# Kernel tuning notes

Hardware: AMD Instinct MI355X
Metric: run time of the kernel (lower is better)

## Reference

```python
import jax, jax.numpy as jnp
import numpy as np
import math

N = 2048       # num_nodes (dense graph)
F_IN = 256     # num_in_features
F_OUT = 256    # num_out_features
H = 8          # num_heads
LN_EPS = 1e-5

# NOTE: every e3nn FullyConnectedTensorProduct in this module maps
# (Fx0e) x irreps_sh -> (Kx0e). Only the l=0 spherical-harmonic component can
# couple scalars to scalars, and Y_0 = 1 under normalization='component'.
# Each TP is therefore exactly a linear map with a 1/sqrt(fan_in) path norm,
# and edge_direction does not enter the math at all.


def setup_inputs() -> dict:
    key = jax.random.key(0)
    ks = jax.random.split(key, 12)
    inv = 1.0 / np.sqrt(F_IN)
    return {
        "node_features": jax.random.normal(ks[0], (N, F_IN), jnp.float32),
        "edges_features_distance": jax.random.uniform(ks[1], (N, N), jnp.float32),
        "edges_features_bond": jax.random.uniform(ks[2], (N, N), jnp.float32),
        "edge_direction": jax.random.normal(ks[3], (N * N, 3), jnp.float32),
        "degree_matrix": jax.random.randint(ks[4], (N, N), 0, 2).astype(jnp.float32),
        # tensor-product weights (xavier-ish scale)
        "Wq": jax.random.normal(ks[5], (F_IN, H), jnp.float32) * inv,
        "Wk": jax.random.normal(ks[6], (F_IN, H), jnp.float32) * inv,
        "Wv": jax.random.normal(ks[7], (F_IN, F_OUT), jnp.float32) * inv,
        "w_bond": jax.random.normal(ks[8], (), jnp.float32),
        "w_bond_contrib": jax.random.normal(ks[9], (), jnp.float32),
        "w_gauss": jax.random.normal(ks[10], (), jnp.float32),
    }


def reference(node_features, edges_features_distance, edges_features_bond,
              edge_direction, degree_matrix, Wq, Wk, Wv,
              w_bond, w_bond_contrib, w_gauss):
    scale = 1.0 / jnp.sqrt(jnp.asarray(F_IN, node_features.dtype))
    # scalar-only tensor products == scaled linears (Y_0 = 1)
    q = (node_features @ Wq) * scale              # [N, H]
    k = (node_features @ Wk) * scale              # [N, H]
    v = (node_features @ Wv) * scale              # [N, F_OUT]

    # raw_attention[i,j,h] = (q_i + k_i)/sqrt(H)  (key.transpose(0,1) picks node i)
    qk = (q + k) / math.sqrt(H)                   # [N, H]
    bond = edges_features_bond * (w_bond * w_bond_contrib)   # [N, N]
    gauss = edges_features_distance * w_gauss                 # [N, N]
    raw = qk[:, None, :] + (bond + gauss)[:, :, None]          # [N, N, H]

    mask = jnp.where(degree_matrix > 0, 0.0, -1e9).astype(raw.dtype)
    scores = jax.nn.leaky_relu(raw, 0.2) + mask[:, :, None]
    # torch F.softmax without dim on a 3-D tensor -> dim=0
    attn = jax.nn.softmax(scores, axis=0)          # [N, N, H]
    # F.dropout treated as identity (eval / deterministic baseline)
    attn_mean = attn.mean(axis=2)                  # [N, N]

    # aggregated[i] = sum_j attn_mean[i,j] * v_j  (value[i,j,:] = v(node_j))
    aggregated = attn_mean @ v                     # [N, F_OUT]
    updated_nodes = jax.nn.elu(aggregated)

    # no_grad connectivity update
    un = jax.lax.stop_gradient(updated_nodes)
    sim = un @ un.T                                # [N, N]
    dd = -jax.lax.stop_gradient(edges_features_distance)
    conn = jax.nn.sigmoid(sim) * dd * jax.lax.stop_gradient(degree_matrix)
    mu = conn.mean(axis=-1, keepdims=True)
    var = conn.var(axis=-1, keepdims=True)
    conn = (conn - mu) * jax.lax.rsqrt(var + LN_EPS)
    conn = conn + conn.T
    return updated_nodes, conn
```

## Files before the change

### kernel.cpp

```cpp
#include <hip/hip_runtime.h>
#include <hip/hip_bf16.h>

#define NN 2048
#define FIN 256
#define FOUT 256
#define HH 8

typedef short bhalf8 __attribute__((ext_vector_type(8)));
typedef float f32x4  __attribute__((ext_vector_type(4)));

__device__ __forceinline__ unsigned short f2b(float f) {
    __hip_bfloat16 h = __float2bfloat16(f);
    return *reinterpret_cast<unsigned short*>(&h);
}
__device__ __forceinline__ float b2f(unsigned short u) {
    __hip_bfloat16 h = *reinterpret_cast<__hip_bfloat16*>(&u);
    return __bfloat162float(h);
}

__global__ __launch_bounds__(256) void k1_qkv(
    const float* __restrict__ x, const float* __restrict__ Wq,
    const float* __restrict__ Wk, const float* __restrict__ Wv,
    float* __restrict__ v, float* __restrict__ qk)
{
    const int ib = blockIdx.x * 4;
    const int t  = threadIdx.x;
    __shared__ float xs[4][FIN];
    __shared__ float part[256];
    #pragma unroll
    for (int n = 0; n < 4; ++n) xs[n][t] = x[(long)(ib+n)*FIN + t];
    __syncthreads();
    float a0 = 0.f, a1 = 0.f, a2 = 0.f, a3 = 0.f;
    #pragma unroll 4
    for (int c = 0; c < FIN; ++c) {
        const float wv = Wv[c*FOUT + t];
        a0 = fmaf(xs[0][c], wv, a0); a1 = fmaf(xs[1][c], wv, a1);
        a2 = fmaf(xs[2][c], wv, a2); a3 = fmaf(xs[3][c], wv, a3);
    }
    v[(ib+0)*FOUT + t] = a0 * 0.0625f;
    v[(ib+1)*FOUT + t] = a1 * 0.0625f;
    v[(ib+2)*FOUT + t] = a2 * 0.0625f;
    v[(ib+3)*FOUT + t] = a3 * 0.0625f;
    {
        const int n = t >> 6, h = t & 7, seg = (t >> 3) & 7;
        float a = 0.f;
        for (int c = seg*32; c < seg*32 + 32; ++c)
            a = fmaf(xs[n][c], Wq[c*HH + h] + Wk[c*HH + h], a);
        part[t] = a;
    }
    __syncthreads();
    if (t < 32) {
        const int n = t >> 3, h = t & 7;
        float a = 0.f;
        #pragma unroll
        for (int s2 = 0; s2 < 8; ++s2) a += part[n*64 + s2*8 + h];
        qk[(ib+n)*HH + h] = a * (0.0625f * 0.35355339059327373f);
    }
}

__global__ __launch_bounds__(256) void k1b_vT(
    const float* __restrict__ v, unsigned short* __restrict__ vtb)
{
    const int k0 = blockIdx.x * 64;
    const int f0 = blockIdx.y * 64;
    const int t  = threadIdx.x;
    __shared__ float LT[64][68];
    const int r  = t >> 4;
    const int c4 = (t & 15) * 4;
    #pragma unroll
    for (int p = 0; p < 4; ++p) {
        const float4 q = *(const float4*)&v[(k0 + r + p*16)*FOUT + f0 + c4];
        LT[c4+0][r + p*16] = q.x; LT[c4+1][r + p*16] = q.y;
        LT[c4+2][r + p*16] = q.z; LT[c4+3][r + p*16] = q.w;
    }
    __syncthreads();
    #pragma unroll
    for (int p = 0; p < 4; ++p) {
        const int fr = r + p*16;
        ushort4 ub;
        ub.x = f2b(LT[fr][c4+0]); ub.y = f2b(LT[fr][c4+1]);
        ub.z = f2b(LT[fr][c4+2]); ub.w = f2b(LT[fr][c4+3]);
        *(ushort4*)&vtb[(long)(f0 + fr)*NN + k0 + c4] = ub;
    }
}

__global__ __launch_bounds__(256) void k2_denom(
    const float* __restrict__ bond, const float* __restrict__ dist,
    const float* __restrict__ deg, const float* __restrict__ qk,
    const float* __restrict__ wb, const float* __restrict__ wbc,
    const float* __restrict__ wg, float* __restrict__ D,
    unsigned short* __restrict__ fbuf, unsigned short* __restrict__ ddb)
{
    const float cb = wb[0] * wbc[0];
    const float cg = wg[0];
    const int t  = threadIdx.x;
    const int tx = t & 63;
    const int ty = t >> 6;
    const int j0 = blockIdx.x * 256;
    const int i0 = blockIdx.y * 64;
    const int j  = j0 + tx*4;
    __shared__ float qs[64*8];
    __shared__ float red[4][2048];
    for (int p = t; p < 512; p += 256) qs[p] = qk[i0*8 + p];
    __syncthreads();
    float acc[4][8];
    #pragma unroll
    for (int jj = 0; jj < 4; ++jj)
        #pragma unroll
        for (int h = 0; h < 8; ++h) acc[jj][h] = 0.f;
    const int ibase = i0 + ty*16;
    for (int ii = 0; ii < 16; ++ii) {
        const long idx = (long)(ibase + ii)*NN + j;
        const float4 dv = *(const float4*)&dist[idx];
        const float4 bv = *(const float4*)&bond[idx];
        const float4 gv = *(const float4*)&deg[idx];
        ushort4 fb, db;
        fb.x = f2b((gv.x > 0.f) ? fmaf(cb, bv.x, cg*dv.x) : -__builtin_inff());
        fb.y = f2b((gv.y > 0.f) ? fmaf(cb, bv.y, cg*dv.y) : -__builtin_inff());
        fb.z = f2b((gv.z > 0.f) ? fmaf(cb, bv.z, cg*dv.z) : -__builtin_inff());
        fb.w = f2b((gv.w > 0.f) ? fmaf(cb, bv.w, cg*dv.w) : -__builtin_inff());
        db.x = f2b(-dv.x * gv.x); db.y = f2b(-dv.y * gv.y);
        db.z = f2b(-dv.z * gv.z); db.w = f2b(-dv.w * gv.w);
        *(ushort4*)&fbuf[idx] = fb;
        *(ushort4*)&ddb[idx]  = db;
        float s[4];
        s[0] = b2f(fb.x); s[1] = b2f(fb.y); s[2] = b2f(fb.z); s[3] = b2f(fb.w);
        const float* qrow = &qs[(ty*16 + ii)*8];
        #pragma unroll
        for (int h = 0; h < 8; ++h) {
            const float q = qrow[h];
            #pragma unroll
            for (int jj = 0; jj < 4; ++jj) {
                float r = q + s[jj];
                r = fmaxf(r, 0.2f*r);
                acc[jj][h] += __expf(r);
            }
        }
    }
    #pragma unroll
    for (int jj = 0; jj < 4; ++jj)
        #pragma unroll
        for (int h = 0; h < 8; ++h) red[ty][(tx*4 + jj)*8 + h] = acc[jj][h];
    __syncthreads();
    for (int p = t; p < 2048; p += 256) {
        const float ssum = red[0][p] + red[1][p] + red[2][p] + red[3][p];
        atomicAdd(&D[j0*8 + p], ssum);
    }
}

__global__ __launch_bounds__(256) void k3_attnmean(
    const unsigned short* __restrict__ fbuf, const float* __restrict__ qk,
    const float* __restrict__ D, unsigned short* __restrict__ amb)
{
    const int t  = threadIdx.x;
    const int tx = t & 63;
    const int ty = t >> 6;
    const int j0 = blockIdx.x * 256;
    const int i0 = blockIdx.y * 64;
    const int j  = j0 + tx*4;
    __shared__ float qs[64*8];
    for (int p = t; p < 512; p += 256) qs[p] = qk[i0*8 + p];
    __syncthreads();
    float invD[4][8];
    #pragma unroll
    for (int jj = 0; jj < 4; ++jj) {
        const float4 d0 = *(const float4*)&D[(j + jj)*8 + 0];
        const float4 d1 = *(const float4*)&D[(j + jj)*8 + 4];
        invD[jj][0] = 0.125f / fmaxf(d0.x, 1e-30f);
        invD[jj][1] = 0.125f / fmaxf(d0.y, 1e-30f);
        invD[jj][2] = 0.125f / fmaxf(d0.z, 1e-30f);
        invD[jj][3] = 0.125f / fmaxf(d0.w, 1e-30f);
        invD[jj][4] = 0.125f / fmaxf(d1.x, 1e-30f);
        invD[jj][5] = 0.125f / fmaxf(d1.y, 1e-30f);
        invD[jj][6] = 0.125f / fmaxf(d1.z, 1e-30f);
        invD[jj][7] = 0.125f / fmaxf(d1.w, 1e-30f);
    }
    const int ibase = i0 + ty*16;
    for (int ii = 0; ii < 16; ++ii) {
        const long idx = (long)(ibase + ii)*NN + j;
        const ushort4 fb = *(const ushort4*)&fbuf[idx];
        float s[4];
        s[0] = b2f(fb.x); s[1] = b2f(fb.y); s[2] = b2f(fb.z); s[3] = b2f(fb.w);
        float o[4] = {0.f, 0.f, 0.f, 0.f};
        const float* qrow = &qs[(ty*16 + ii)*8];
        #pragma unroll
        for (int h = 0; h < 8; ++h) {
            const float q = qrow[h];
            #pragma unroll
            for (int jj = 0; jj < 4; ++jj) {
                float r = q + s[jj];
                r = fmaxf(r, 0.2f*r);
                o[jj] = fmaf(__expf(r), invD[jj][h], o[jj]);
            }
        }
        ushort4 ob;
        ob.x = f2b(o[0]); ob.y = f2b(o[1]); ob.z = f2b(o[2]); ob.w = f2b(o[3]);
        *(ushort4*)&amb[idx] = ob;
    }
}

__global__ __launch_bounds__(128) void k4_aggr(
    const unsigned short* __restrict__ amb,
    const unsigned short* __restrict__ vtb,
    float* __restrict__ out0, unsigned short* __restrict__ unb)
{
    const int i0 = blockIdx.x * 32;
    const int f0 = blockIdx.y * 32;
    const int w  = threadIdx.x >> 6;
    const int l  = threadIdx.x & 63;
    const int lm = l & 15, lq = l >> 4;
    const int iw = i0 + w*16;
    f32x4 acc0 = {0,0,0,0}, acc1 = {0,0,0,0};
    const unsigned short* arow  = &amb[(long)(iw + lm)*NN + lq*8];
    const unsigned short* brow0 = &vtb[(long)(f0 + lm)*NN + lq*8];
    const unsigned short* brow1 = &vtb[(long)(f0 + 16 + lm)*NN + lq*8];
    #pragma unroll 4
    for (int kk = 0; kk < NN; kk += 32) {
        const bhalf8 a  = *(const bhalf8*)&arow[kk];
        const bhalf8 b0 = *(const bhalf8*)&brow0[kk];
        const bhalf8 b1 = *(const bhalf8*)&brow1[kk];
        acc0 = __builtin_amdgcn_mfma_f32_16x16x32_bf16(a, b0, acc0, 0, 0, 0);
        acc1 = __builtin_amdgcn_mfma_f32_16x16x32_bf16(a, b1, acc1, 0, 0, 0);
    }
    #pragma unroll
    for (int r = 0; r < 4; ++r) {
        const int i = iw + lq*4 + r;
        float s0 = acc0[r], s1 = acc1[r];
        s0 = (s0 > 0.f) ? s0 : (__expf(s0) - 1.f);
        s1 = (s1 > 0.f) ? s1 : (__expf(s1) - 1.f);
        out0[(long)i*FOUT + f0 + lm]      = s0;
        out0[(long)i*FOUT + f0 + 16 + lm] = s1;
        unb[(long)i*FOUT + f0 + lm]       = f2b(s0);
        unb[(long)i*FOUT + f0 + 16 + lm]  = f2b(s1);
    }
}

__global__ __launch_bounds__(256) void k5_sim(
    const unsigned short* __restrict__ unb, const unsigned short* __restrict__ ddb,
    unsigned short* __restrict__ c0,
    float* __restrict__ rowsum, float* __restrict__ rowsq)
{
    const int i0 = blockIdx.y * 64;
    const int j0 = blockIdx.x * 64;
    const int w  = threadIdx.x >> 6;
    const int l  = threadIdx.x & 63;
    const int lm = l & 15, lq = l >> 4;
    const int iw = i0 + w*16;
    f32x4 acc[4] = {f32x4{0,0,0,0}, f32x4{0,0,0,0}, f32x4{0,0,0,0}, f32x4{0,0,0,0}};
    for (int kk = 0; kk < FOUT; kk += 32) {
        const bhalf8 a = *(const bhalf8*)&unb[(long)(iw + lm)*FOUT + kk + lq*8];
        #pragma unroll
        for (int c = 0; c < 4; ++c) {
            const bhalf8 b = *(const bhalf8*)&unb[(long)(j0 + c*16 + lm)*FOUT + kk + lq*8];
            acc[c] = __builtin_amdgcn_mfma_f32_16x16x32_bf16(a, b, acc[c], 0, 0, 0);
        }
    }
    float srow[4] = {0.f,0.f,0.f,0.f}, qrow[4] = {0.f,0.f,0.f,0.f};
    #pragma unroll
    for (int c = 0; c < 4; ++c) {
        #pragma unroll
        for (int r = 0; r < 4; ++r) {
            const int i = iw + lq*4 + r;
            const int j = j0 + c*16 + lm;
            const long idx = (long)i*NN + j;
            const float sg = 1.f / (1.f + __expf(-acc[c][r]));
            const float val = sg * b2f(ddb[idx]);
            c0[idx] = f2b(val);
            srow[r] += val;
            qrow[r] = fmaf(val, val, qrow[r]);
        }
    }
    #pragma unroll
    for (int r = 0; r < 4; ++r) {
        #pragma unroll
        for (int m = 8; m >= 1; m >>= 1) {
            srow[r] += __shfl_xor(srow[r], m, 64);
            qrow[r] += __shfl_xor(qrow[r], m, 64);
        }
        if (lm == 0) {
            atomicAdd(&rowsum[iw + lq*4 + r], srow[r]);
            atomicAdd(&rowsq[iw + lq*4 + r],  qrow[r]);
        }
    }
}

__global__ void k6_stats(const float* __restrict__ rowsum,
                         const float* __restrict__ rowsq,
                         float* __restrict__ mu, float* __restrict__ rs)
{
    const int i = blockIdx.x*256 + threadIdx.x;
    if (i < NN) {
        const float m = rowsum[i] * (1.f/NN);
        const float var = rowsq[i] * (1.f/NN) - m*m;
        mu[i] = m;
        rs[i] = rsqrtf(var + 1e-5f);
    }
}

__global__ __launch_bounds__(256) void k7_conn(
    const unsigned short* __restrict__ c0, const float* __restrict__ mu,
    const float* __restrict__ rs, float* __restrict__ out1)
{
    const int i0 = blockIdx.y * 64;
    const int j0 = blockIdx.x * 64;
    const int t  = threadIdx.x;
    __shared__ float LT[64][68];
    __shared__ float muj[64], rsj[64];
    const int r  = t >> 4;
    const int c4 = (t & 15) * 4;
    if (t < 64)        muj[t] = mu[j0 + t];
    else if (t < 128)  rsj[t-64] = rs[j0 + t - 64];
    #pragma unroll
    for (int p = 0; p < 4; ++p) {
        const int jl = r + p*16;
        const ushort4 q = *(const ushort4*)&c0[(long)(j0 + jl)*NN + i0 + c4];
        LT[c4+0][jl] = b2f(q.x); LT[c4+1][jl] = b2f(q.y);
        LT[c4+2][jl] = b2f(q.z); LT[c4+3][jl] = b2f(q.w);
    }
    __syncthreads();
    #pragma unroll
    for (int p = 0; p < 4; ++p) {
        const int rr = r + p*16;
        const int i  = i0 + rr;
        const ushort4 xb = *(const ushort4*)&c0[(long)i*NN + j0 + c4];
        const float mi = mu[i], ri = rs[i];
        float4 o;
        o.x = (b2f(xb.x) - mi)*ri + (LT[rr][c4+0] - muj[c4+0])*rsj[c4+0];
        o.y = (b2f(xb.y) - mi)*ri + (LT[rr][c4+1] - muj[c4+1])*rsj[c4+1];
        o.z = (b2f(xb.z) - mi)*ri + (LT[rr][c4+2] - muj[c4+2])*rsj[c4+2];
        o.w = (b2f(xb.w) - mi)*ri + (LT[rr][c4+3] - muj[c4+3])*rsj[c4+3];
        *(float4*)&out1[(long)i*NN + j0 + c4] = o;
    }
}

extern "C" void kernel_launch(void* const* d_in, const int* in_sizes, int n_in,
                              void* d_out, int out_size, void* d_ws, size_t ws_size,
                              hipStream_t stream)
{
    const float* x    = (const float*)d_in[0];
    const float* dist = (const float*)d_in[1];
    const float* bond = (const float*)d_in[2];
    const float* deg  = (const float*)d_in[4];
    const float* Wq   = (const float*)d_in[5];
    const float* Wk   = (const float*)d_in[6];
    const float* Wv   = (const float*)d_in[7];
    const float* wb   = (const float*)d_in[8];
    const float* wbc  = (const float*)d_in[9];
    const float* wg   = (const float*)d_in[10];

    float* out0 = (float*)d_out;
    float* out1 = out0 + (size_t)NN*FOUT;

    char* w = (char*)d_ws;
    unsigned short* fbuf = (unsigned short*)(w);
    unsigned short* c0   = (unsigned short*)(w);
    unsigned short* amb  = (unsigned short*)(w +  8388608);
    unsigned short* ddb  = (unsigned short*)(w + 16777216);
    float* v       = (float*)(w + 33554432);
    unsigned short* vtb = (unsigned short*)(w + 35651584);
    unsigned short* unb = (unsigned short*)(w + 36700160);
    float* qk      = (float*)(w + 37748736);
    float* D       = (float*)(w + 37814272);
    float* rowsum  = (float*)(w + 37879808);
    float* rowsq   = (float*)(w + 37888000);
    float* mu      = (float*)(w + 37896192);
    float* rs      = (float*)(w + 37904384);

    hipMemsetAsync(D, 0, 65536 + 8192 + 8192, stream);

    k1_qkv<<<NN/4, 256, 0, stream>>>(x, Wq, Wk, Wv, v, qk);
    dim3 g1b(NN/64, FOUT/64);
    k1b_vT<<<g1b, 256, 0, stream>>>(v, vtb);
    dim3 g23(NN/256, NN/64);
    k2_denom<<<g23, 256, 0, stream>>>(bond, dist, deg, qk, wb, wbc, wg, D, fbuf, ddb);
    k3_attnmean<<<g23, 256, 0, stream>>>(fbuf, qk, D, amb);
    dim3 g4(NN/32, FOUT/32);
    k4_aggr<<<g4, 128, 0, stream>>>(amb, vtb, out0, unb);
    dim3 g5(NN/64, NN/64);
    k5_sim<<<g5, 256, 0, stream>>>(unb, ddb, c0, rowsum, rowsq);
    k6_stats<<<8, 256, 0, stream>>>(rowsum, rowsq, mu, rs);
    k7_conn<<<g5, 256, 0, stream>>>(c0, mu, rs, out1);
}
```

Measured before the change: 250.8 us.

## Fuse all stages into one persistent kernel with grid-wide barriers

Replaces the eight separate kernel launches with a single persistent kernel of 256 blocks × 1024 threads that runs each stage in turn, separated by atomic-counter grid barriers. It also writes v directly as transposed bf16, dropping the transpose kernel and its buffer, zeroes the accumulators inside the kernel, and folds the stats kernel into the final normalize stage. The aim is to remove launch gaps and intermediate traffic. In exchange, every stage is limited to a fixed grid and pays barrier spin costs, and correctness depends on all 256 blocks being resident at once.

```diff
diff --git a/kernel.cpp b/kernel.cpp
--- a/kernel.cpp
+++ b/kernel.cpp
@@ -5,6 +5,8 @@
 #define FIN 256
 #define FOUT 256
 #define HH 8
+#define NB 256
+#define NT 1024
 
 typedef short bhalf8 __attribute__((ext_vector_type(8)));
 typedef float f32x4  __attribute__((ext_vector_type(4)));
@@ -18,318 +20,309 @@
     return __bfloat162float(h);
 }
 
-__global__ __launch_bounds__(256) void k1_qkv(
-    const float* __restrict__ x, const float* __restrict__ Wq,
-    const float* __restrict__ Wk, const float* __restrict__ Wv,
-    float* __restrict__ v, float* __restrict__ qk)
+__device__ __forceinline__ void gridbar(unsigned* bar, unsigned target) {
+    __syncthreads();
+    if (threadIdx.x == 0) {
+        __threadfence();
+        __hip_atomic_fetch_add(bar, 1u, __ATOMIC_ACQ_REL, __HIP_MEMORY_SCOPE_AGENT);
+        while (__hip_atomic_load(bar, __ATOMIC_ACQUIRE, __HIP_MEMORY_SCOPE_AGENT) < target) {
+            __builtin_amdgcn_s_sleep(8);
+        }
+        __threadfence();
+    }
+    __syncthreads();
+}
+
+union SharedU {
+    struct { float xs[4][4][256]; float part[4][256]; } p1;
+    struct { float qs[512]; float red[4][4][16][4][8]; } p2;
+    struct { float qs[512]; } p3;
+    struct { float LT[64][68]; float mui[64], rii[64], muj[64], rsj[64]; } p7;
+};
+
+__global__ __launch_bounds__(NT, 4) void mega(
+    const float* __restrict__ x,    const float* __restrict__ dist,
+    const float* __restrict__ bond, const float* __restrict__ deg,
+    const float* __restrict__ Wq,   const float* __restrict__ Wk,
+    const float* __restrict__ Wv,   const float* __restrict__ wb,
+    const float* __restrict__ wbc,  const float* __restrict__ wg,
+    float* __restrict__ out0, float* __restrict__ out1,
+    unsigned short* __restrict__ fbuf_c0,
+    unsigned short* __restrict__ amb, unsigned short* __restrict__ ddb,
+    unsigned short* __restrict__ vtb, unsigned short* __restrict__ unb,
+    float* __restrict__ qk, float* __restrict__ D,
+    float* __restrict__ rowsum, float* __restrict__ rowsq,
+    unsigned* __restrict__ bar)
 {
-    const int ib = blockIdx.x * 4;
-    const int t  = threadIdx.x;
-    __shared__ float xs[4][FIN];
-    __shared__ float part[256];
-    #pragma unroll
-    for (int n = 0; n < 4; ++n) xs[n][t] = x[(long)(ib+n)*FIN + t];
-    __syncthreads();
-    float a0 = 0.f, a1 = 0.f, a2 = 0.f, a3 = 0.f;
-    #pragma unroll 4
-    for (int c = 0; c < FIN; ++c) {
-        const float wv = Wv[c*FOUT + t];
-        a0 = fmaf(xs[0][c], wv, a0); a1 = fmaf(xs[1][c], wv, a1);
-        a2 = fmaf(xs[2][c], wv, a2); a3 = fmaf(xs[3][c], wv, a3);
-    }
-    v[(ib+0)*FOUT + t] = a0 * 0.0625f;
-    v[(ib+1)*FOUT + t] = a1 * 0.0625f;
-    v[(ib+2)*FOUT + t] = a2 * 0.0625f;
-    v[(ib+3)*FOUT + t] = a3 * 0.0625f;
+    __shared__ SharedU sh;
+    const int gid = blockIdx.x;
+    const int tid = threadIdx.x;
+
+    if (gid < 128) {
+        const int g = tid >> 8, sub = tid & 255;
+        const int ib = (gid*4 + g) * 4;
+        float (*xs)[256] = sh.p1.xs[g];
+        #pragma unroll
+        for (int n = 0; n < 4; ++n) xs[n][sub] = x[(long)(ib+n)*FIN + sub];
+        __syncthreads();
+        float a0 = 0.f, a1 = 0.f, a2 = 0.f, a3 = 0.f;
+        #pragma unroll 4
+        for (int c = 0; c < FIN; ++c) {
+            const float wv = Wv[c*FOUT + sub];
+            a0 = fmaf(xs[0][c], wv, a0); a1 = fmaf(xs[1][c], wv, a1);
+            a2 = fmaf(xs[2][c], wv, a2); a3 = fmaf(xs[3][c], wv, a3);
+        }
+        ushort4 uv;
+        uv.x = f2b(a0 * 0.0625f); uv.y = f2b(a1 * 0.0625f);
+        uv.z = f2b(a2 * 0.0625f); uv.w = f2b(a3 * 0.0625f);
+        *(ushort4*)&vtb[(long)sub*NN + ib] = uv;
+        {
+            const int n = sub >> 6, h = sub & 7, seg = (sub >> 3) & 7;
+            float a = 0.f;
+            for (int c = seg*32; c < seg*32 + 32; ++c)
+                a = fmaf(xs[n][c], Wq[c*HH + h] + Wk[c*HH + h], a);
+            sh.p1.part[g][sub] = a;
+        }
+        __syncthreads();
+        if (sub < 32) {
+            const int n = sub >> 3, h = sub & 7;
+            float a = 0.f;
+            #pragma unroll
+            for (int s2 = 0; s2 < 8; ++s2) a += sh.p1.part[g][n*64 + s2*8 + h];
+            qk[(ib+n)*HH + h] = a * (0.0625f * 0.35355339059327373f);
+        }
+    } else {
+        const int tp = (gid - 128)*NT + tid;
+        if      (tp < 16384) D[tp] = 0.f;
+        else if (tp < 18432) rowsum[tp - 16384] = 0.f;
+        else if (tp < 20480) rowsq [tp - 18432] = 0.f;
+    }
+    gridbar(bar, NB*1);
+
     {
-        const int n = t >> 6, h = t & 7, seg = (t >> 3) & 7;
-        float a = 0.f;
-        for (int c = seg*32; c < seg*32 + 32; ++c)
-            a = fmaf(xs[n][c], Wq[c*HH + h] + Wk[c*HH + h], a);
-        part[t] = a;
-    }
-    __syncthreads();
-    if (t < 32) {
-        const int n = t >> 3, h = t & 7;
-        float a = 0.f;
-        #pragma unroll
-        for (int s2 = 0; s2 < 8; ++s2) a += part[n*64 + s2*8 + h];
-        qk[(ib+n)*HH + h] = a * (0.0625f * 0.35355339059327373f);
-    }
-}
-
-__global__ __launch_bounds__(256) void k1b_vT(
-    const float* __restrict__ v, unsigned short* __restrict__ vtb)
-{
-    const int k0 = blockIdx.x * 64;
-    const int f0 = blockIdx.y * 64;
-    const int t  = threadIdx.x;
-    __shared__ float LT[64][68];
-    const int r  = t >> 4;
-    const int c4 = (t & 15) * 4;
-    #pragma unroll
-    for (int p = 0; p < 4; ++p) {
-        const float4 q = *(const float4*)&v[(k0 + r + p*16)*FOUT + f0 + c4];
-        LT[c4+0][r + p*16] = q.x; LT[c4+1][r + p*16] = q.y;
-        LT[c4+2][r + p*16] = q.z; LT[c4+3][r + p*16] = q.w;
-    }
-    __syncthreads();
-    #pragma unroll
-    for (int p = 0; p < 4; ++p) {
-        const int fr = r + p*16;
-        ushort4 ub;
-        ub.x = f2b(LT[fr][c4+0]); ub.y = f2b(LT[fr][c4+1]);
-        ub.z = f2b(LT[fr][c4+2]); ub.w = f2b(LT[fr][c4+3]);
-        *(ushort4*)&vtb[(long)(f0 + fr)*NN + k0 + c4] = ub;
-    }
-}
-
-__global__ __launch_bounds__(256) void k2_denom(
-    const float* __restrict__ bond, const float* __restrict__ dist,
-    const float* __restrict__ deg, const float* __restrict__ qk,
-    const float* __restrict__ wb, const float* __restrict__ wbc,
-    const float* __restrict__ wg, float* __restrict__ D,
-    unsigned short* __restrict__ fbuf, unsigned short* __restrict__ ddb)
-{
-    const float cb = wb[0] * wbc[0];
-    const float cg = wg[0];
-    const int t  = threadIdx.x;
-    const int tx = t & 63;
-    const int ty = t >> 6;
-    const int j0 = blockIdx.x * 256;
-    const int i0 = blockIdx.y * 64;
-    const int j  = j0 + tx*4;
-    __shared__ float qs[64*8];
-    __shared__ float red[4][2048];
-    for (int p = t; p < 512; p += 256) qs[p] = qk[i0*8 + p];
-    __syncthreads();
-    float acc[4][8];
-    #pragma unroll
-    for (int jj = 0; jj < 4; ++jj)
-        #pragma unroll
-        for (int h = 0; h < 8; ++h) acc[jj][h] = 0.f;
-    const int ibase = i0 + ty*16;
-    for (int ii = 0; ii < 16; ++ii) {
-        const long idx = (long)(ibase + ii)*NN + j;
-        const float4 dv = *(const float4*)&dist[idx];
-        const float4 bv = *(const float4*)&bond[idx];
-        const float4 gv = *(const float4*)&deg[idx];
-        ushort4 fb, db;
-        fb.x = f2b((gv.x > 0.f) ? fmaf(cb, bv.x, cg*dv.x) : -__builtin_inff());
-        fb.y = f2b((gv.y > 0.f) ? fmaf(cb, bv.y, cg*dv.y) : -__builtin_inff());
-        fb.z = f2b((gv.z > 0.f) ? fmaf(cb, bv.z, cg*dv.z) : -__builtin_inff());
-        fb.w = f2b((gv.w > 0.f) ? fmaf(cb, bv.w, cg*dv.w) : -__builtin_inff());
-        db.x = f2b(-dv.x * gv.x); db.y = f2b(-dv.y * gv.y);
-        db.z = f2b(-dv.z * gv.z); db.w = f2b(-dv.w * gv.w);
-        *(ushort4*)&fbuf[idx] = fb;
-        *(ushort4*)&ddb[idx]  = db;
-        float s[4];
-        s[0] = b2f(fb.x); s[1] = b2f(fb.y); s[2] = b2f(fb.z); s[3] = b2f(fb.w);
-        const float* qrow = &qs[(ty*16 + ii)*8];
-        #pragma unroll
-        for (int h = 0; h < 8; ++h) {
-            const float q = qrow[h];
-            #pragma unroll
-            for (int jj = 0; jj < 4; ++jj) {
-                float r = q + s[jj];
-                r = fmaxf(r, 0.2f*r);
-                acc[jj][h] += __expf(r);
-            }
-        }
-    }
-    #pragma unroll
-    for (int jj = 0; jj < 4; ++jj)
-        #pragma unroll
-        for (int h = 0; h < 8; ++h) red[ty][(tx*4 + jj)*8 + h] = acc[jj][h];
-    __syncthreads();
-    for (int p = t; p < 2048; p += 256) {
-        const float ssum = red[0][p] + red[1][p] + red[2][p] + red[3][p];
-        atomicAdd(&D[j0*8 + p], ssum);
-    }
-}
-
-__global__ __launch_bounds__(256) void k3_attnmean(
-    const unsigned short* __restrict__ fbuf, const float* __restrict__ qk,
-    const float* __restrict__ D, unsigned short* __restrict__ amb)
-{
-    const int t  = threadIdx.x;
-    const int tx = t & 63;
-    const int ty = t >> 6;
-    const int j0 = blockIdx.x * 256;
-    const int i0 = blockIdx.y * 64;
-    const int j  = j0 + tx*4;
-    __shared__ float qs[64*8];
-    for (int p = t; p < 512; p += 256) qs[p] = qk[i0*8 + p];
-    __syncthreads();
-    float invD[4][8];
-    #pragma unroll
-    for (int jj = 0; jj < 4; ++jj) {
-        const float4 d0 = *(const float4*)&D[(j + jj)*8 + 0];
-        const float4 d1 = *(const float4*)&D[(j + jj)*8 + 4];
-        invD[jj][0] = 0.125f / fmaxf(d0.x, 1e-30f);
-        invD[jj][1] = 0.125f / fmaxf(d0.y, 1e-30f);
-        invD[jj][2] = 0.125f / fmaxf(d0.z, 1e-30f);
-        invD[jj][3] = 0.125f / fmaxf(d0.w, 1e-30f);
-        invD[jj][4] = 0.125f / fmaxf(d1.x, 1e-30f);
-        invD[jj][5] = 0.125f / fmaxf(d1.y, 1e-30f);
-        invD[jj][6] = 0.125f / fmaxf(d1.z, 1e-30f);
-        invD[jj][7] = 0.125f / fmaxf(d1.w, 1e-30f);
-    }
-    const int ibase = i0 + ty*16;
-    for (int ii = 0; ii < 16; ++ii) {
-        const long idx = (long)(ibase + ii)*NN + j;
-        const ushort4 fb = *(const ushort4*)&fbuf[idx];
-        float s[4];
-        s[0] = b2f(fb.x); s[1] = b2f(fb.y); s[2] = b2f(fb.z); s[3] = b2f(fb.w);
-        float o[4] = {0.f, 0.f, 0.f, 0.f};
-        const float* qrow = &qs[(ty*16 + ii)*8];
-        #pragma unroll
-        for (int h = 0; h < 8; ++h) {
-            const float q = qrow[h];
-            #pragma unroll
-            for (int jj = 0; jj < 4; ++jj) {
-                float r = q + s[jj];
-                r = fmaxf(r, 0.2f*r);
-                o[jj] = fmaf(__expf(r), invD[jj][h], o[jj]);
-            }
-        }
-        ushort4 ob;
-        ob.x = f2b(o[0]); ob.y = f2b(o[1]); ob.z = f2b(o[2]); ob.w = f2b(o[3]);
-        *(ushort4*)&amb[idx] = ob;
-    }
-}
-
-__global__ __launch_bounds__(128) void k4_aggr(
-    const unsigned short* __restrict__ amb,
-    const unsigned short* __restrict__ vtb,
-    float* __restrict__ out0, unsigned short* __restrict__ unb)
-{
-    const int i0 = blockIdx.x * 32;
-    const int f0 = blockIdx.y * 32;
-    const int w  = threadIdx.x >> 6;
-    const int l  = threadIdx.x & 63;
-    const int lm = l & 15, lq = l >> 4;
-    const int iw = i0 + w*16;
-    f32x4 acc0 = {0,0,0,0}, acc1 = {0,0,0,0};
-    const unsigned short* arow  = &amb[(long)(iw + lm)*NN + lq*8];
-    const unsigned short* brow0 = &vtb[(long)(f0 + lm)*NN + lq*8];
-    const unsigned short* brow1 = &vtb[(long)(f0 + 16 + lm)*NN + lq*8];
-    #pragma unroll 4
-    for (int kk = 0; kk < NN; kk += 32) {
-        const bhalf8 a  = *(const bhalf8*)&arow[kk];
-        const bhalf8 b0 = *(const bhalf8*)&brow0[kk];
-        const bhalf8 b1 = *(const bhalf8*)&brow1[kk];
-        acc0 = __builtin_amdgcn_mfma_f32_16x16x32_bf16(a, b0, acc0, 0, 0, 0);
-        acc1 = __builtin_amdgcn_mfma_f32_16x16x32_bf16(a, b1, acc1, 0, 0, 0);
-    }
-    #pragma unroll
-    for (int r = 0; r < 4; ++r) {
-        const int i = iw + lq*4 + r;
-        float s0 = acc0[r], s1 = acc1[r];
-        s0 = (s0 > 0.f) ? s0 : (__expf(s0) - 1.f);
-        s1 = (s1 > 0.f) ? s1 : (__expf(s1) - 1.f);
-        out0[(long)i*FOUT + f0 + lm]      = s0;
-        out0[(long)i*FOUT + f0 + 16 + lm] = s1;
-        unb[(long)i*FOUT + f0 + lm]       = f2b(s0);
-        unb[(long)i*FOUT + f0 + 16 + lm]  = f2b(s1);
-    }
-}
-
-__global__ __launch_bounds__(256) void k5_sim(
-    const unsigned short* __restrict__ unb, const unsigned short* __restrict__ ddb,
-    unsigned short* __restrict__ c0,
-    float* __restrict__ rowsum, float* __restrict__ rowsq)
-{
-    const int i0 = blockIdx.y * 64;
-    const int j0 = blockIdx.x * 64;
-    const int w  = threadIdx.x >> 6;
-    const int l  = threadIdx.x & 63;
-    const int lm = l & 15, lq = l >> 4;
-    const int iw = i0 + w*16;
-    f32x4 acc[4] = {f32x4{0,0,0,0}, f32x4{0,0,0,0}, f32x4{0,0,0,0}, f32x4{0,0,0,0}};
-    for (int kk = 0; kk < FOUT; kk += 32) {
-        const bhalf8 a = *(const bhalf8*)&unb[(long)(iw + lm)*FOUT + kk + lq*8];
+        const float cb = wb[0] * wbc[0];
+        const float cg = wg[0];
+        const int bx = gid & 7, by = gid >> 3;
+        const int j0 = bx*256, i0 = by*64;
+        const int w  = tid >> 6, lane = tid & 63;
+        const int jb = w & 3,  tqh = w >> 2;
+        const int jq = lane & 15, tql = lane >> 4;
+        const int tq = tqh*4 + tql;
+        const int j  = j0 + (jb*16 + jq)*4;
+        if (tid < 512) sh.p2.qs[tid] = qk[i0*8 + tid];
+        __syncthreads();
+        float acc[4][8];
+        #pragma unroll
+        for (int jj = 0; jj < 4; ++jj)
+            #pragma unroll
+            for (int h = 0; h < 8; ++h) acc[jj][h] = 0.f;
+        #pragma unroll
+        for (int ii = 0; ii < 4; ++ii) {
+            const int i = i0 + tq*4 + ii;
+            const long idx = (long)i*NN + j;
+            const float4 dv = *(const float4*)&dist[idx];
+            const float4 bv = *(const float4*)&bond[idx];
+            const float4 gv = *(const float4*)&deg[idx];
+            ushort4 fb, db;
+            fb.x = f2b((gv.x > 0.f) ? fmaf(cb, bv.x, cg*dv.x) : -__builtin_inff());
+            fb.y = f2b((gv.y > 0.f) ? fmaf(cb, bv.y, cg*dv.y) : -__builtin_inff());
+            fb.z = f2b((gv.z > 0.f) ? fmaf(cb, bv.z, cg*dv.z) : -__builtin_inff());
+            fb.w = f2b((gv.w > 0.f) ? fmaf(cb, bv.w, cg*dv.w) : -__builtin_inff());
+            db.x = f2b(-dv.x * gv.x); db.y = f2b(-dv.y * gv.y);
+            db.z = f2b(-dv.z * gv.z); db.w = f2b(-dv.w * gv.w);
+            *(ushort4*)&fbuf_c0[idx] = fb;
+            *(ushort4*)&ddb[idx]     = db;
+            float s[4];
+            s[0] = b2f(fb.x); s[1] = b2f(fb.y); s[2] = b2f(fb.z); s[3] = b2f(fb.w);
+            const float* qrow = &sh.p2.qs[(tq*4 + ii)*8];
+            #pragma unroll
+            for (int h = 0; h < 8; ++h) {
+                const float q = qrow[h];
+                #pragma unroll
+                for (int jj = 0; jj < 4; ++jj) {
+                    float r = q + s[jj];
+                    r = fmaxf(r, 0.2f*r);
+                    acc[jj][h] += __expf(r);
+                }
+            }
+        }
+        #pragma unroll
+        for (int jj = 0; jj < 4; ++jj)
+            #pragma unroll
+            for (int h = 0; h < 8; ++h) {
+                float v = acc[jj][h];
+                v += __shfl_xor(v, 16, 64);
+                v += __shfl_xor(v, 32, 64);
+                acc[jj][h] = v;
+            }
+        if (tql == 0) {
+            #pragma unroll
+            for (int jj = 0; jj < 4; ++jj)
+                #pragma unroll
+                for (int h = 0; h < 8; ++h)
+                    sh.p2.red[tqh][jb][jq][jj][h] = acc[jj][h];
+        }
+        __syncthreads();
+        for (int p = tid; p < 2048; p += NT) {
+            const int jl = p >> 3, h = p & 7;
+            const int q4 = jl >> 2, jj = jl & 3;
+            const int jb2 = q4 >> 4, jq2 = q4 & 15;
+            const float ssum = sh.p2.red[0][jb2][jq2][jj][h] + sh.p2.red[1][jb2][jq2][jj][h]
+                             + sh.p2.red[2][jb2][jq2][jj][h] + sh.p2.red[3][jb2][jq2][jj][h];
+            atomicAdd(&D[(j0 + jl)*8 + h], ssum);
+        }
+    }
+    gridbar(bar, NB*2);
+
+    {
+        const int bx = gid & 7, by = gid >> 3;
+        const int j0 = bx*256, i0 = by*64;
+        const int w  = tid >> 6, lane = tid & 63;
+        const int jb = w & 3,  tqh = w >> 2;
+        const int jq = lane & 15, tql = lane >> 4;
+        const int tq = tqh*4 + tql;
+        const int j  = j0 + (jb*16 + jq)*4;
+        if (tid < 512) sh.p3.qs[tid] = qk[i0*8 + tid];
+        __syncthreads();
+        float invD[4][8];
+        #pragma unroll
+        for (int jj = 0; jj < 4; ++jj)
+            #pragma unroll
+            for (int h = 0; h < 8; ++h)
+                invD[jj][h] = 0.125f / fmaxf(D[(j + jj)*8 + h], 1e-30f);
+        #pragma unroll
+        for (int ii = 0; ii < 4; ++ii) {
+            const int i = i0 + tq*4 + ii;
+            const long idx = (long)i*NN + j;
+            const ushort4 fb = *(const ushort4*)&fbuf_c0[idx];
+            float s[4];
+            s[0] = b2f(fb.x); s[1] = b2f(fb.y); s[2] = b2f(fb.z); s[3] = b2f(fb.w);
+            float o[4] = {0.f, 0.f, 0.f, 0.f};
+            const float* qrow = &sh.p3.qs[(tq*4 + ii)*8];
+            #pragma unroll
+            for (int h = 0; h < 8; ++h) {
+                const float q = qrow[h];
+                #pragma unroll
+                for (int jj = 0; jj < 4; ++jj) {
+                    float r = q + s[jj];
+                    r = fmaxf(r, 0.2f*r);
+                    o[jj] = fmaf(__expf(r), invD[jj][h], o[jj]);
+                }
+            }
+            ushort4 ob;
+            ob.x = f2b(o[0]); ob.y = f2b(o[1]); ob.z = f2b(o[2]); ob.w = f2b(o[3]);
+            *(ushort4*)&amb[idx] = ob;
+        }
+    }
+    gridbar(bar, NB*3);
+
+    {
+        const int w = tid >> 6, lane = tid & 63;
+        const int vw = gid*16 + w;
+        if (vw < 2048) {
+            const int it = vw >> 4;
+            const int f0 = (vw & 15) * 16;
+            const int lm = lane & 15, lq = lane >> 4;
+            const unsigned short* arow = &amb[(long)(it*16 + lm)*NN + lq*8];
+            const unsigned short* brow = &vtb[(long)(f0 + lm)*NN + lq*8];
+            f32x4 acc = {0.f, 0.f, 0.f, 0.f};
+            #pragma unroll 4
+            for (int kk = 0; kk < NN; kk += 32) {
+                const bhalf8 a = *(const bhalf8*)&arow[kk];
+                const bhalf8 b = *(const bhalf8*)&brow[kk];
+                acc = __builtin_amdgcn_mfma_f32_16x16x32_bf16(a, b, acc, 0, 0, 0);
+            }
+            #pragma unroll
+            for (int r = 0; r < 4; ++r) {
+                const int i = it*16 + lq*4 + r;
+                const int f = f0 + lm;
+                float s = acc[r];
+                s = (s > 0.f) ? s : (__expf(s) - 1.f);
+                out0[(long)i*FOUT + f] = s;
+                unb [(long)i*FOUT + f] = f2b(s);
+            }
+        }
+    }
+    gridbar(bar, NB*4);
+
+    {
+        const int vb = gid*4 + (tid >> 8);
+        const int vt = tid & 255;
+        const int i0 = (vb >> 5)*64, j0 = (vb & 31)*64;
+        const int w2 = vt >> 6, l = vt & 63;
+        const int lm = l & 15, lq = l >> 4;
+        const int iw = i0 + w2*16;
+        f32x4 acc[4] = {f32x4{0,0,0,0}, f32x4{0,0,0,0}, f32x4{0,0,0,0}, f32x4{0,0,0,0}};
+        for (int kk = 0; kk < FOUT; kk += 32) {
+            const bhalf8 a = *(const bhalf8*)&unb[(long)(iw + lm)*FOUT + kk + lq*8];
+            #pragma unroll
+            for (int c = 0; c < 4; ++c) {
+                const bhalf8 b = *(const bhalf8*)&unb[(long)(j0 + c*16 + lm)*FOUT + kk + lq*8];
+                acc[c] = __builtin_amdgcn_mfma_f32_16x16x32_bf16(a, b, acc[c], 0, 0, 0);
+            }
+        }
+        float srow[4] = {0.f,0.f,0.f,0.f}, qrow[4] = {0.f,0.f,0.f,0.f};
         #pragma unroll
         for (int c = 0; c < 4; ++c) {
-            const bhalf8 b = *(const bhalf8*)&unb[(long)(j0 + c*16 + lm)*FOUT + kk + lq*8];
-            acc[c] = __builtin_amdgcn_mfma_f32_16x16x32_bf16(a, b, acc[c], 0, 0, 0);
-        }
-    }
-    float srow[4] = {0.f,0.f,0.f,0.f}, qrow[4] = {0.f,0.f,0.f,0.f};
-    #pragma unroll
-    for (int c = 0; c < 4; ++c) {
+            #pragma unroll
+            for (int r = 0; r < 4; ++r) {
+                const int i = iw + lq*4 + r;
+                const int j = j0 + c*16 + lm;
+                const long idx = (long)i*NN + j;
+                const float sg = 1.f / (1.f + __expf(-acc[c][r]));
+                const float val = sg * b2f(ddb[idx]);
+                fbuf_c0[idx] = f2b(val);
+                srow[r] += val;
+                qrow[r] = fmaf(val, val, qrow[r]);
+            }
+        }
         #pragma unroll
         for (int r = 0; r < 4; ++r) {
-            const int i = iw + lq*4 + r;
-            const int j = j0 + c*16 + lm;
-            const long idx = (long)i*NN + j;
-            const float sg = 1.f / (1.f + __expf(-acc[c][r]));
-            const float val = sg * b2f(ddb[idx]);
-            c0[idx] = f2b(val);
-            srow[r] += val;
-            qrow[r] = fmaf(val, val, qrow[r]);
-        }
-    }
-    #pragma unroll
-    for (int r = 0; r < 4; ++r) {
-        #pragma unroll
-        for (int m = 8; m >= 1; m >>= 1) {
-            srow[r] += __shfl_xor(srow[r], m, 64);
-            qrow[r] += __shfl_xor(qrow[r], m, 64);
-        }
-        if (lm == 0) {
-            atomicAdd(&rowsum[iw + lq*4 + r], srow[r]);
-            atomicAdd(&rowsq[iw + lq*4 + r],  qrow[r]);
-        }
-    }
-}
-
-__global__ void k6_stats(const float* __restrict__ rowsum,
-                         const float* __restrict__ rowsq,
-                         float* __restrict__ mu, float* __restrict__ rs)
-{
-    const int i = blockIdx.x*256 + threadIdx.x;
-    if (i < NN) {
-        const float m = rowsum[i] * (1.f/NN);
-        const float var = rowsq[i] * (1.f/NN) - m*m;
-        mu[i] = m;
-        rs[i] = rsqrtf(var + 1e-5f);
-    }
-}
-
-__global__ __launch_bounds__(256) void k7_conn(
-    const unsigned short* __restrict__ c0, const float* __restrict__ mu,
-    const float* __restrict__ rs, float* __restrict__ out1)
-{
-    const int i0 = blockIdx.y * 64;
-    const int j0 = blockIdx.x * 64;
-    const int t  = threadIdx.x;
-    __shared__ float LT[64][68];
-    __shared__ float muj[64], rsj[64];
-    const int r  = t >> 4;
-    const int c4 = (t & 15) * 4;
-    if (t < 64)        muj[t] = mu[j0 + t];
-    else if (t < 128)  rsj[t-64] = rs[j0 + t - 64];
-    #pragma unroll
-    for (int p = 0; p < 4; ++p) {
-        const int jl = r + p*16;
-        const ushort4 q = *(const ushort4*)&c0[(long)(j0 + jl)*NN + i0 + c4];
-        LT[c4+0][jl] = b2f(q.x); LT[c4+1][jl] = b2f(q.y);
-        LT[c4+2][jl] = b2f(q.z); LT[c4+3][jl] = b2f(q.w);
-    }
-    __syncthreads();
-    #pragma unroll
-    for (int p = 0; p < 4; ++p) {
-        const int rr = r + p*16;
-        const int i  = i0 + rr;
-        const ushort4 xb = *(const ushort4*)&c0[(long)i*NN + j0 + c4];
-        const float mi = mu[i], ri = rs[i];
-        float4 o;
-        o.x = (b2f(xb.x) - mi)*ri + (LT[rr][c4+0] - muj[c4+0])*rsj[c4+0];
-        o.y = (b2f(xb.y) - mi)*ri + (LT[rr][c4+1] - muj[c4+1])*rsj[c4+1];
-        o.z = (b2f(xb.z) - mi)*ri + (LT[rr][c4+2] - muj[c4+2])*rsj[c4+2];
-        o.w = (b2f(xb.w) - mi)*ri + (LT[rr][c4+3] - muj[c4+3])*rsj[c4+3];
-        *(float4*)&out1[(long)i*NN + j0 + c4] = o;
+            #pragma unroll
+            for (int m = 8; m >= 1; m >>= 1) {
+                srow[r] += __shfl_xor(srow[r], m, 64);
+                qrow[r] += __shfl_xor(qrow[r], m, 64);
+            }
+            if (lm == 0) {
+                atomicAdd(&rowsum[iw + lq*4 + r], srow[r]);
+                atomicAdd(&rowsq [iw + lq*4 + r], qrow[r]);
+            }
+        }
+    }
+    gridbar(bar, NB*5);
+
+    for (int tile = gid; tile < 1024; tile += NB) {
+        const int i0 = (tile >> 5)*64, j0 = (tile & 31)*64;
+        __syncthreads();
+        if (tid < 64) {
+            const float m = rowsum[j0 + tid] * (1.f/NN);
+            sh.p7.muj[tid] = m;
+            sh.p7.rsj[tid] = rsqrtf(rowsq[j0 + tid]*(1.f/NN) - m*m + 1e-5f);
+        } else if (tid < 128) {
+            const int rr = tid - 64;
+            const float m = rowsum[i0 + rr] * (1.f/NN);
+            sh.p7.mui[rr] = m;
+            sh.p7.rii[rr] = rsqrtf(rowsq[i0 + rr]*(1.f/NN) - m*m + 1e-5f);
+        }
+        const int r  = tid >> 4;
+        const int c4 = (tid & 15) * 4;
+        {
+            const ushort4 q = *(const ushort4*)&fbuf_c0[(long)(j0 + r)*NN + i0 + c4];
+            sh.p7.LT[c4+0][r] = b2f(q.x); sh.p7.LT[c4+1][r] = b2f(q.y);
+            sh.p7.LT[c4+2][r] = b2f(q.z); sh.p7.LT[c4+3][r] = b2f(q.w);
+        }
+        __syncthreads();
+        {
+            const int i = i0 + r;
+            const ushort4 xb = *(const ushort4*)&fbuf_c0[(long)i*NN + j0 + c4];
+            const float mi = sh.p7.mui[r], ri = sh.p7.rii[r];
+            float4 o;
+            o.x = (b2f(xb.x) - mi)*ri + (sh.p7.LT[r][c4+0] - sh.p7.muj[c4+0])*sh.p7.rsj[c4+0];
+            o.y = (b2f(xb.y) - mi)*ri + (sh.p7.LT[r][c4+1] - sh.p7.muj[c4+1])*sh.p7.rsj[c4+1];
+            o.z = (b2f(xb.z) - mi)*ri + (sh.p7.LT[r][c4+2] - sh.p7.muj[c4+2])*sh.p7.rsj[c4+2];
+            o.w = (b2f(xb.w) - mi)*ri + (sh.p7.LT[r][c4+3] - sh.p7.muj[c4+3])*sh.p7.rsj[c4+3];
+            *(float4*)&out1[(long)i*NN + j0 + c4] = o;
+        }
     }
 }
 
@@ -352,32 +345,19 @@
     float* out1 = out0 + (size_t)NN*FOUT;
 
     char* w = (char*)d_ws;
-    unsigned short* fbuf = (unsigned short*)(w);
-    unsigned short* c0   = (unsigned short*)(w);
+    unsigned short* fbuf_c0 = (unsigned short*)(w);
     unsigned short* amb  = (unsigned short*)(w +  8388608);
     unsigned short* ddb  = (unsigned short*)(w + 16777216);
-    float* v       = (float*)(w + 33554432);
-    unsigned short* vtb = (unsigned short*)(w + 35651584);
-    unsigned short* unb = (unsigned short*)(w + 36700160);
+    unsigned short* vtb  = (unsigned short*)(w + 35651584);
+    unsigned short* unb  = (unsigned short*)(w + 36700160);
     float* qk      = (float*)(w + 37748736);
     float* D       = (float*)(w + 37814272);
     float* rowsum  = (float*)(w + 37879808);
     float* rowsq   = (float*)(w + 37888000);
-    float* mu      = (float*)(w + 37896192);
-    float* rs      = (float*)(w + 37904384);
-
-    hipMemsetAsync(D, 0, 65536 + 8192 + 8192, stream);
-
-    k1_qkv<<<NN/4, 256, 0, stream>>>(x, Wq, Wk, Wv, v, qk);
-    dim3 g1b(NN/64, FOUT/64);
-    k1b_vT<<<g1b, 256, 0, stream>>>(v, vtb);
-    dim3 g23(NN/256, NN/64);
-    k2_denom<<<g23, 256, 0, stream>>>(bond, dist, deg, qk, wb, wbc, wg, D, fbuf, ddb);
-    k3_attnmean<<<g23, 256, 0, stream>>>(fbuf, qk, D, amb);
-    dim3 g4(NN/32, FOUT/32);
-    k4_aggr<<<g4, 128, 0, stream>>>(amb, vtb, out0, unb);
-    dim3 g5(NN/64, NN/64);
-    k5_sim<<<g5, 256, 0, stream>>>(unb, ddb, c0, rowsum, rowsq);
-    k6_stats<<<8, 256, 0, stream>>>(rowsum, rowsq, mu, rs);
-    k7_conn<<<g5, 256, 0, stream>>>(c0, mu, rs, out1);
-}
+    unsigned* bar  = (unsigned*)(w + 37896192);
+
+    hipMemsetAsync(bar, 0, 128, stream);
+    hipLaunchKernelGGL(mega, dim3(NB), dim3(NT), 0, stream,
+        x, dist, bond, deg, Wq, Wk, Wv, wb, wbc, wg,
+        out0, out1, fbuf_c0, amb, ddb, vtb, unb, qk, D, rowsum, rowsq, bar);
+}
```

Result: slower. 535.6 us (+113.6%).
